# Kernel optimization log

Measured on AMD Instinct MI355X. Metric: run time of the kernel, lower is better.

Reference implementation:

```python
import jax, jax.numpy as jnp
import numpy as np

jax.config.update("jax_enable_x64", True)  # hash math needs int64 (prime * coord > 2^31)

LEVEL = 16
MOD_T = 2 ** 16
FDIM = 3
_PRIMES = (1, 2654435761, 805459861)  # first feature_dim primes from the module


def _grid_sizes():
    # mirrors torch float32 computation: b = exp((log(n_max)-log(n_min))/(level-1))
    n_min = np.float32(4.0)
    n_max = np.float32(256.0)
    b = np.float32(np.exp((np.log(n_max) - np.log(n_min)) / np.float32(LEVEL - 1)))
    return [int(n_min * b ** i) for i in range(LEVEL)]


def setup_inputs() -> dict:
    key = jax.random.key(0)
    k1, k2 = jax.random.split(key)
    images = jax.random.uniform(k1, (16, 3, 256, 256), dtype=jnp.float32)
    hash_table = (jax.random.uniform(k2, (LEVEL, MOD_T, FDIM), dtype=jnp.float32)
                  * 0.0002 - 0.0001)
    return {"images": images, "hash_table": hash_table}


def reference(images, hash_table):
    b, c, h, w = images.shape
    primes = jnp.array(_PRIMES[:FDIM], dtype=jnp.int64)
    neg_inf = jnp.array(-jnp.inf, dtype=images.dtype)
    outs = []
    for lvl, grid in enumerate(_grid_sizes()):
        kh, kw = h // grid, w // grid
        # max_pool2d(images*grid, kernel=(kh,kw), stride=(kh,kw))
        pooled = jax.lax.reduce_window(
            images * grid, neg_inf, jax.lax.max,
            window_dimensions=(1, 1, kh, kw),
            window_strides=(1, 1, kh, kw),
            padding="VALID")                     # [B, F, gh, gw]
        idx = pooled.astype(jnp.int64) * primes[None, :, None, None]
        g = idx[:, 0]
        for i in range(1, FDIM):
            g = g ^ idx[:, i]
        g = g % MOD_T                             # [B, gh, gw]
        f = hash_table[lvl][g]                    # gather -> [B, gh, gw, F]
        f = jnp.transpose(f, (0, 3, 1, 2))        # [B, F, gh, gw]
        # F.interpolate(..., mode='bilinear') == half-pixel, align_corners=False
        f = jax.image.resize(f, (b, FDIM, h, w), method="bilinear")
        outs.append(f)
    return jnp.concatenate(outs, axis=1)          # [B, level*F, H, W]
```

## Files before the change

### kernel.cpp

```cpp
#include <hip/hip_runtime.h>
#include <stdint.h>
#include <math.h>


#define NLVL 16
#define NB   16

__constant__ int   c_P[NLVL]   = {4,5,6,9,12,15,21,28,36,51,64,85,128,256,256,256};
__constant__ float c_G[NLVL]   = {4.f,5.f,6.f,9.f,12.f,15.f,21.f,27.f,36.f,48.f,63.f,84.f,111.f,147.f,194.f,255.f};
__constant__ int   c_CUM[14]   = {0,16,41,77,158,302,527,968,1752,3048,5649,9745,16970,33354};

#define CELLS_PB   33354
#define CELLS_TOT  (CELLS_PB*NB)
#define MWS_FLOATS (CELLS_TOT*3)
#define POOL_BLOCKS (NB*32)
#define HG_BLOCKS  ((CELLS_TOT+255)/256)
#define DIR_BLOCKS  1024
#define TILE_BLOCKS (13*16*16)
#define K3_BLOCKS   (DIR_BLOCKS + TILE_BLOCKS)

__device__ __forceinline__ uint32_t hash3(float m0, float m1, float m2, float g) {
    uint32_t v0 = (uint32_t)(int)(m0 * g);
    uint32_t v1 = (uint32_t)(int)(m1 * g);
    uint32_t v2 = (uint32_t)(int)(m2 * g);
    return (v0 ^ (v1 * 2654435761u) ^ (v2 * 805459861u)) & 0xFFFFu;
}

__global__ __launch_bounds__(256) void zero_mws(float4* __restrict__ mws4)
{
    int t = blockIdx.x * 256 + threadIdx.x;
    if (t < MWS_FLOATS / 4) mws4[t] = make_float4(0.f, 0.f, 0.f, 0.f);
}

__global__ __launch_bounds__(256) void pool_single(const float* __restrict__ img,
                                                   unsigned int* __restrict__ mws)
{
    static constexpr int K_P[13]   = {4,5,6,9,12,15,21,28,36,51,64,85,128};
    static constexpr int K_KH[13]  = {64,51,42,28,21,17,12,9,7,5,4,3,2};
    static constexpr int K_CUM[13] = {0,16,41,77,158,302,527,968,1752,3048,5649,9745,16970};

    __shared__ float simg[3][8][256];
    __shared__ float colbuf[3][256];

    int b    = blockIdx.x >> 5;
    int band = blockIdx.x & 31;
    int y0   = band * 8;

    const float* base = img + (size_t)b * 196608 + (size_t)y0 * 256;
    for (int t = threadIdx.x; t < 1536; t += 256) {
        int ch = t >> 9;
        int r  = t & 511;
        float4 v = *(const float4*)(base + (size_t)ch * 65536 + r * 4);
        int row = r >> 6, c4 = (r & 63) << 2;
        simg[ch][row][c4 + 0] = v.x;
        simg[ch][row][c4 + 1] = v.y;
        simg[ch][row][c4 + 2] = v.z;
        simg[ch][row][c4 + 3] = v.w;
    }
    __syncthreads();

    int x = threadIdx.x;
#pragma unroll
    for (int lvl = 0; lvl < 13; ++lvl) {
        const int kh = K_KH[lvl], P = K_P[lvl];
        int nr0 = y0 / kh;
        int nr1 = (y0 + 7) / kh; if (nr1 > P - 1) nr1 = P - 1;
        for (int cr = nr0; cr <= nr1; ++cr) {
            int rlo = cr * kh;      if (rlo < y0) rlo = y0;
            int rhi = cr * kh + kh; if (rhi > y0 + 8) rhi = y0 + 8;
            float p0 = -INFINITY, p1 = -INFINITY, p2 = -INFINITY;
            for (int r = rlo; r < rhi; ++r) {
                int rr = r - y0;
                p0 = fmaxf(p0, simg[0][rr][x]);
                p1 = fmaxf(p1, simg[1][rr][x]);
                p2 = fmaxf(p2, simg[2][rr][x]);
            }
            colbuf[0][x] = p0; colbuf[1][x] = p1; colbuf[2][x] = p2;
            __syncthreads();
            if (x < P) {
                float q0 = -INFINITY, q1 = -INFINITY, q2 = -INFINITY;
                for (int c = x * kh; c < x * kh + kh; ++c) {
                    q0 = fmaxf(q0, colbuf[0][c]);
                    q1 = fmaxf(q1, colbuf[1][c]);
                    q2 = fmaxf(q2, colbuf[2][c]);
                }
                int idx = K_CUM[lvl] * NB + b * P * P + cr * P + x;
                atomicMax(&mws[idx],                 __float_as_uint(q0));
                atomicMax(&mws[idx + CELLS_TOT],     __float_as_uint(q1));
                atomicMax(&mws[idx + 2 * CELLS_TOT], __float_as_uint(q2));
            }
            __syncthreads();
        }
    }
}

__global__ __launch_bounds__(256) void hashgather(const float* __restrict__ mws,
                                                  const float* __restrict__ tab,
                                                  float* __restrict__ fws)
{
    static constexpr int K_CUM16[13] = {0,256,656,1232,2528,4832,8432,15488,28032,48768,90384,155920,271520};
    int tid = blockIdx.x * 256 + threadIdx.x;
    if (tid >= CELLS_TOT) return;
    int lvl = 0;
#pragma unroll
    for (int l = 1; l < 13; ++l) lvl += (tid >= K_CUM16[l]);
    float m0 = mws[tid];
    float m1 = mws[tid + CELLS_TOT];
    float m2 = mws[tid + 2 * CELLS_TOT];
    uint32_t g = hash3(m0, m1, m2, c_G[lvl]);
    float3 tv = *(const float3*)(tab + (size_t)lvl * 196608 + g * 3);
    float4 fv; fv.x = tv.x; fv.y = tv.y; fv.z = tv.z; fv.w = 0.f;
    *(float4*)(fws + (size_t)tid * 4) = fv;
}

__global__ __launch_bounds__(256) void render(const float* __restrict__ img,
                                              const float* __restrict__ tab,
                                              const float* __restrict__ fws,
                                              float* __restrict__ out)
{
    __shared__ float4 s[34 * 34];
    if (blockIdx.x < DIR_BLOCKS) {
        int t = blockIdx.x * 256 + threadIdx.x;
        int b = t >> 14;
        int pix0 = (t & 16383) << 2;
        const float* p = img + (size_t)b * 196608 + pix0;
        float4 i0 = *(const float4*)p;
        float4 i1 = *(const float4*)(p + 65536);
        float4 i2 = *(const float4*)(p + 131072);
#pragma unroll
        for (int lvl = 13; lvl < 16; ++lvl) {
            float g = c_G[lvl];
            const float* T = tab + (size_t)lvl * 196608;
            uint32_t g0 = hash3(i0.x, i1.x, i2.x, g);
            uint32_t g1 = hash3(i0.y, i1.y, i2.y, g);
            uint32_t g2 = hash3(i0.z, i1.z, i2.z, g);
            uint32_t g3 = hash3(i0.w, i1.w, i2.w, g);
            float3 f0 = *(const float3*)(T + g0 * 3);
            float3 f1 = *(const float3*)(T + g1 * 3);
            float3 f2 = *(const float3*)(T + g2 * 3);
            float3 f3 = *(const float3*)(T + g3 * 3);
            float4 o0, o1, o2;
            o0.x = f0.x; o1.x = f0.y; o2.x = f0.z;
            o0.y = f1.x; o1.y = f1.y; o2.y = f1.z;
            o0.z = f2.x; o1.z = f2.y; o2.z = f2.z;
            o0.w = f3.x; o1.w = f3.y; o2.w = f3.z;
            float* ob = out + ((size_t)b * 48 + 3 * lvl) * 65536 + pix0;
            *(float4*)ob            = o0;
            *(float4*)(ob + 65536)  = o1;
            *(float4*)(ob + 131072) = o2;
        }
        return;
    }

    int blk   = blockIdx.x - DIR_BLOCKS;
    int tile  = blk & 15;
    int plane = blk >> 4;
    int lvl   = plane >> 4;
    int b     = plane & 15;
    int P     = c_P[lvl];
    int yt0   = (tile >> 2) * 64;
    int xt0   = (tile & 3) * 64;

    int nlo  = ((2 * yt0 + 1) * P - 256) >> 9;
    int r_lo = nlo < 0 ? 0 : (nlo > P - 1 ? P - 1 : nlo);
    int nhi  = (((2 * (yt0 + 63) + 1) * P - 256) >> 9) + 1;
    int r_hi = nhi < 0 ? 0 : (nhi > P - 1 ? P - 1 : nhi);
    int mlo  = ((2 * xt0 + 1) * P - 256) >> 9;
    int c_lo = mlo < 0 ? 0 : (mlo > P - 1 ? P - 1 : mlo);
    int mhi  = (((2 * (xt0 + 63) + 1) * P - 256) >> 9) + 1;
    int c_hi = mhi < 0 ? 0 : (mhi > P - 1 ? P - 1 : mhi);
    int span_y = r_hi - r_lo + 1;
    int span_x = c_hi - c_lo + 1;

    const float4* fb4 = (const float4*)fws + (size_t)c_CUM[lvl] * NB + (size_t)b * P * P;
    int n = span_y * span_x;
    for (int t = threadIdx.x; t < n; t += 256) {
        int r = t / span_x, c = t - r * span_x;
        s[t] = fb4[(size_t)(r_lo + r) * P + c_lo + c];
    }
    __syncthreads();

    int lane = threadIdx.x & 63;
    int w    = threadIdx.x >> 6;
    int xq   = lane & 15;
    int rg   = lane >> 4;
    int xb   = xt0 + xq * 4;

    int ix0t[4], ix1t[4]; float wx1t[4];
#pragma unroll
    for (int j = 0; j < 4; ++j) {
        int numx = (2 * (xb + j) + 1) * P - 256;
        int ix0  = numx >> 9;
        float fx = (float)(numx & 511) * (1.0f / 512.0f);
        int ix1;
        if (ix0 < 0)           { ix0 = 0;     ix1 = 0;     fx = 0.f; }
        else if (ix0 >= P - 1) { ix0 = P - 1; ix1 = P - 1; fx = 0.f; }
        else                   { ix1 = ix0 + 1; }
        ix0t[j] = ix0 - c_lo; ix1t[j] = ix1 - c_lo; wx1t[j] = fx;
    }

#pragma unroll
    for (int k = 0; k < 4; ++k) {
        int y = yt0 + w * 16 + rg * 4 + k;
        int numy = (2 * y + 1) * P - 256;
        int iy0  = numy >> 9;
        float fy = (float)(numy & 511) * (1.0f / 512.0f);
        int iy1;
        if (iy0 < 0)           { iy0 = 0;     iy1 = 0;     fy = 0.f; }
        else if (iy0 >= P - 1) { iy0 = P - 1; iy1 = P - 1; fy = 0.f; }
        else                   { iy1 = iy0 + 1; }
        const float4* p0 = s + (iy0 - r_lo) * span_x;
        const float4* p1 = s + (iy1 - r_lo) * span_x;
        float wy1 = fy, wy0 = 1.f - fy;

        float v[3][4];
#pragma unroll
        for (int j = 0; j < 4; ++j) {
            float wx1 = wx1t[j], wx0 = 1.f - wx1;
            float4 t00 = p0[ix0t[j]];
            float4 t01 = p0[ix1t[j]];
            float4 t10 = p1[ix0t[j]];
            float4 t11 = p1[ix1t[j]];
            v[0][j] = wy0 * (wx0 * t00.x + wx1 * t01.x) + wy1 * (wx0 * t10.x + wx1 * t11.x);
            v[1][j] = wy0 * (wx0 * t00.y + wx1 * t01.y) + wy1 * (wx0 * t10.y + wx1 * t11.y);
            v[2][j] = wy0 * (wx0 * t00.z + wx1 * t01.z) + wy1 * (wx0 * t10.z + wx1 * t11.z);
        }
        float* o = out + ((size_t)b * 48 + 3 * lvl) * 65536 + (size_t)y * 256 + xb;
#pragma unroll
        for (int c = 0; c < 3; ++c) {
            float4 q; q.x = v[c][0]; q.y = v[c][1]; q.z = v[c][2]; q.w = v[c][3];
            *(float4*)(o + (size_t)c * 65536) = q;
        }
    }
}

extern "C" void kernel_launch(void* const* d_in, const int* in_sizes, int n_in,
                              void* d_out, int out_size, void* d_ws, size_t ws_size,
                              hipStream_t stream)
{
    const float* img = (const float*)d_in[0];
    const float* tab = (const float*)d_in[1];
    float* out = (float*)d_out;
    float* mws = (float*)d_ws;
    float* fws = mws + MWS_FLOATS;

    hipLaunchKernelGGL(zero_mws,    dim3((MWS_FLOATS/4 + 255)/256), dim3(256), 0, stream, (float4*)mws);
    hipLaunchKernelGGL(pool_single, dim3(POOL_BLOCKS), dim3(256), 0, stream, img, (unsigned int*)mws);
    hipLaunchKernelGGL(hashgather,  dim3(HG_BLOCKS), dim3(256), 0, stream, mws, tab, fws);
    hipLaunchKernelGGL(render,      dim3(K3_BLOCKS), dim3(256), 0, stream, img, tab, fws, out);
}
```

Before: 84.03 us.

## Fuse hash-gather into render tile staging and replace zero kernel with memset

Removes the separate hashgather kernel. Each render tile block now reads the pooled maxima directly, computes the hash and gathers the table entries into shared memory itself. The zeroing kernel is replaced by hipMemsetAsync. This saves one launch and the round trip of the intermediate feature buffer through global memory. In exchange, cells shared by neighbouring tiles are hashed and gathered more than once.

Result: no change. 82.49 us (-1.8%).

```diff
diff --git a/kernel.cpp b/kernel.cpp
--- a/kernel.cpp
+++ b/kernel.cpp
@@ -14,22 +14,15 @@
 #define CELLS_TOT  (CELLS_PB*NB)
 #define MWS_FLOATS (CELLS_TOT*3)
 #define POOL_BLOCKS (NB*32)
-#define HG_BLOCKS  ((CELLS_TOT+255)/256)
 #define DIR_BLOCKS  1024
 #define TILE_BLOCKS (13*16*16)
-#define K3_BLOCKS   (DIR_BLOCKS + TILE_BLOCKS)
+#define K2_BLOCKS   (DIR_BLOCKS + TILE_BLOCKS)
 
 __device__ __forceinline__ uint32_t hash3(float m0, float m1, float m2, float g) {
     uint32_t v0 = (uint32_t)(int)(m0 * g);
     uint32_t v1 = (uint32_t)(int)(m1 * g);
     uint32_t v2 = (uint32_t)(int)(m2 * g);
     return (v0 ^ (v1 * 2654435761u) ^ (v2 * 805459861u)) & 0xFFFFu;
-}
-
-__global__ __launch_bounds__(256) void zero_mws(float4* __restrict__ mws4)
-{
-    int t = blockIdx.x * 256 + threadIdx.x;
-    if (t < MWS_FLOATS / 4) mws4[t] = make_float4(0.f, 0.f, 0.f, 0.f);
 }
 
 __global__ __launch_bounds__(256) void pool_single(const float* __restrict__ img,
@@ -94,28 +87,9 @@
     }
 }
 
-__global__ __launch_bounds__(256) void hashgather(const float* __restrict__ mws,
-                                                  const float* __restrict__ tab,
-                                                  float* __restrict__ fws)
-{
-    static constexpr int K_CUM16[13] = {0,256,656,1232,2528,4832,8432,15488,28032,48768,90384,155920,271520};
-    int tid = blockIdx.x * 256 + threadIdx.x;
-    if (tid >= CELLS_TOT) return;
-    int lvl = 0;
-#pragma unroll
-    for (int l = 1; l < 13; ++l) lvl += (tid >= K_CUM16[l]);
-    float m0 = mws[tid];
-    float m1 = mws[tid + CELLS_TOT];
-    float m2 = mws[tid + 2 * CELLS_TOT];
-    uint32_t g = hash3(m0, m1, m2, c_G[lvl]);
-    float3 tv = *(const float3*)(tab + (size_t)lvl * 196608 + g * 3);
-    float4 fv; fv.x = tv.x; fv.y = tv.y; fv.z = tv.z; fv.w = 0.f;
-    *(float4*)(fws + (size_t)tid * 4) = fv;
-}
-
 __global__ __launch_bounds__(256) void render(const float* __restrict__ img,
                                               const float* __restrict__ tab,
-                                              const float* __restrict__ fws,
+                                              const float* __restrict__ mws,
                                               float* __restrict__ out)
 {
     __shared__ float4 s[34 * 34];
@@ -172,11 +146,20 @@
     int span_y = r_hi - r_lo + 1;
     int span_x = c_hi - c_lo + 1;
 
-    const float4* fb4 = (const float4*)fws + (size_t)c_CUM[lvl] * NB + (size_t)b * P * P;
+    int planebase = c_CUM[lvl] * NB + b * P * P;
+    const float* T = tab + (size_t)lvl * 196608;
+    float gmul = c_G[lvl];
     int n = span_y * span_x;
     for (int t = threadIdx.x; t < n; t += 256) {
         int r = t / span_x, c = t - r * span_x;
-        s[t] = fb4[(size_t)(r_lo + r) * P + c_lo + c];
+        int idx = planebase + (r_lo + r) * P + c_lo + c;
+        float m0 = mws[idx];
+        float m1 = mws[idx + CELLS_TOT];
+        float m2 = mws[idx + 2 * CELLS_TOT];
+        uint32_t g = hash3(m0, m1, m2, gmul);
+        float3 tv = *(const float3*)(T + g * 3);
+        float4 fv; fv.x = tv.x; fv.y = tv.y; fv.z = tv.z; fv.w = 0.f;
+        s[t] = fv;
     }
     __syncthreads();
 
@@ -242,10 +225,8 @@
     const float* tab = (const float*)d_in[1];
     float* out = (float*)d_out;
     float* mws = (float*)d_ws;
-    float* fws = mws + MWS_FLOATS;
-
-    hipLaunchKernelGGL(zero_mws,    dim3((MWS_FLOATS/4 + 255)/256), dim3(256), 0, stream, (float4*)mws);
+
+    hipMemsetAsync(mws, 0, (size_t)MWS_FLOATS * sizeof(float), stream);
     hipLaunchKernelGGL(pool_single, dim3(POOL_BLOCKS), dim3(256), 0, stream, img, (unsigned int*)mws);
-    hipLaunchKernelGGL(hashgather,  dim3(HG_BLOCKS), dim3(256), 0, stream, mws, tab, fws);
-    hipLaunchKernelGGL(render,      dim3(K3_BLOCKS), dim3(256), 0, stream, img, tab, fws, out);
-}
+    hipLaunchKernelGGL(render,      dim3(K2_BLOCKS), dim3(256), 0, stream, img, tab, mws, out);
+}
```
